# Kernel tuning notes

Measured on AMD Instinct MI355X. Metric: run time of the kernel, lower is better.

Reference implementation:

```python
import jax, jax.numpy as jnp
import numpy as np

N_AGENTS = 8
STATE_DIM = 256
EMBED_DIM = 32
BATCH = 65536


def setup_inputs() -> dict:
    key = jax.random.key(0)
    ks = jax.random.split(key, 12)
    s = 1.0 / np.sqrt(STATE_DIM)
    se = 1.0 / np.sqrt(EMBED_DIM)
    return {
        "agent_qs": jax.random.normal(ks[0], (BATCH, N_AGENTS), dtype=jnp.float32),
        "states": jax.random.normal(ks[1], (BATCH, STATE_DIM), dtype=jnp.float32),
        # hyper_w_1: Linear(state_dim, embed_dim * n_agents)
        "w1_W": jax.random.uniform(ks[2], (STATE_DIM, EMBED_DIM * N_AGENTS), jnp.float32, -s, s),
        "w1_b": jax.random.uniform(ks[3], (EMBED_DIM * N_AGENTS,), jnp.float32, -s, s),
        # hyper_w_final: Linear(state_dim, embed_dim)
        "wf_W": jax.random.uniform(ks[4], (STATE_DIM, EMBED_DIM), jnp.float32, -s, s),
        "wf_b": jax.random.uniform(ks[5], (EMBED_DIM,), jnp.float32, -s, s),
        # hyper_b_1: Linear(state_dim, embed_dim)
        "b1_W": jax.random.uniform(ks[6], (STATE_DIM, EMBED_DIM), jnp.float32, -s, s),
        "b1_b": jax.random.uniform(ks[7], (EMBED_DIM,), jnp.float32, -s, s),
        # V: Linear(state_dim, embed_dim) -> ReLU -> Linear(embed_dim, 1)
        "v1_W": jax.random.uniform(ks[8], (STATE_DIM, EMBED_DIM), jnp.float32, -s, s),
        "v1_b": jax.random.uniform(ks[9], (EMBED_DIM,), jnp.float32, -s, s),
        "v2_W": jax.random.uniform(ks[10], (EMBED_DIM, 1), jnp.float32, -se, se),
        "v2_b": jax.random.uniform(ks[11], (1,), jnp.float32, -se, se),
    }


def reference(agent_qs, states, w1_W, w1_b, wf_W, wf_b, b1_W, b1_b, v1_W, v1_b, v2_W, v2_b):
    B = agent_qs.shape[0]
    # hypernet weights (abs for monotonicity)
    w1 = jnp.abs(states @ w1_W + w1_b).reshape(B, N_AGENTS, EMBED_DIM)   # [B, A, E]
    w_final = jnp.abs(states @ wf_W + wf_b)                               # [B, E]
    b1 = states @ b1_W + b1_b                                             # [B, E]
    # hidden = elu(agent_qs^T w1 + b1): [B,1,A] @ [B,A,E] -> [B,E]
    hidden = jax.nn.elu(jnp.einsum("ba,bae->be", agent_qs, w1) + b1)
    # mixed = hidden @ w_final: [B,1,E] @ [B,E,1] -> [B,1]
    mixed = jnp.sum(hidden * w_final, axis=-1, keepdims=True)             # [B, 1]
    # state value V(s)
    state_value = jax.nn.relu(states @ v1_W + v1_b) @ v2_W + v2_b         # [B, 1]
    return mixed + state_value
```

## Files before the change

kernel.cpp:

```cpp
#include <hip/hip_runtime.h>
#include <math.h>


#define NTILES 22
#define KCHUNKS 8
#define CHUNK_I4 1408

typedef __attribute__((ext_vector_type(8))) short short8;
typedef __attribute__((ext_vector_type(4))) float float4v;

__device__ __forceinline__ unsigned short f2b(float f) {
    unsigned int u = __float_as_uint(f);
    u = u + 0x7fffu + ((u >> 16) & 1u);
    return (unsigned short)(u >> 16);
}

__device__ __forceinline__ void gl2lds16(const unsigned short* g, unsigned short* l) {
    __builtin_amdgcn_global_load_lds(
        (const __attribute__((address_space(1))) unsigned int*)g,
        (__attribute__((address_space(3))) unsigned int*)l,
        16, 0, 0);
}

__global__ void repack_b(const float* __restrict__ w1_W,
                         const float* __restrict__ wf_W,
                         const float* __restrict__ b1_W,
                         const float* __restrict__ v1_W,
                         unsigned short* __restrict__ brep) {
    int idx = blockIdx.x * 256 + threadIdx.x;
    int lane = idx & 63;
    int tt   = idx >> 6;
    int t    = tt % 22;
    int kc   = tt / 22;
    int kbase = kc * 32 + (lane >> 4) * 8;
    int n = t * 16 + (lane & 15);
    short8 frag;
#pragma unroll
    for (int j = 0; j < 8; ++j) {
        int k = kbase + j;
        float val;
        if (n < 256)      val = w1_W[k * 256 + n];
        else if (n < 288) val = wf_W[k * 32 + (n - 256)];
        else if (n < 320) val = b1_W[k * 32 + (n - 288)];
        else              val = v1_W[k * 32 + (n - 320)];
        frag[j] = (short)f2b(val);
    }
    *(short8*)(&brep[idx * 8]) = frag;
}

__global__ void __launch_bounds__(256, 2)
qmix_main(const float* __restrict__ agent_qs,
          const float* __restrict__ states,
          const unsigned short* __restrict__ brep,
          const float* __restrict__ w1_b,
          const float* __restrict__ wf_b,
          const float* __restrict__ b1_b,
          const float* __restrict__ v1_b,
          const float* __restrict__ v2_W,
          const float* __restrict__ v2_b,
          float* __restrict__ out) {
    __shared__ __align__(16) unsigned short wlds[2][NTILES * 64 * 8];

    const int tid  = threadIdx.x;
    const int wave = tid >> 6, lane = tid & 63;
    const int quad = lane >> 4, l16 = lane & 15;
    const int r0 = blockIdx.x * 128 + wave * 32 + l16;
    const float* srow0 = states + (size_t)r0 * 256;
    const float* srow1 = srow0 + 16 * 256;

    for (int s = wave; s < NTILES; s += 4)
        gl2lds16(brep + (size_t)(s * 64 + lane) * 8, wlds[0] + s * 512);

    float4v s0a = *(const float4v*)(srow0 + quad * 8);
    float4v s0b = *(const float4v*)(srow0 + quad * 8 + 4);
    float4v s1a = *(const float4v*)(srow1 + quad * 8);
    float4v s1b = *(const float4v*)(srow1 + quad * 8 + 4);

    float4v acc[2][NTILES];
#pragma unroll
    for (int g = 0; g < 2; ++g)
#pragma unroll
        for (int t = 0; t < NTILES; ++t)
#pragma unroll
            for (int q = 0; q < 4; ++q) acc[g][t][q] = 0.f;

    __syncthreads();

    int cur = 0;
    for (int kc = 0; kc < KCHUNKS; ++kc) {
        if (kc < KCHUNKS - 1) {
            const unsigned short* src = brep + (size_t)(kc + 1) * CHUNK_I4 * 8;
            unsigned short* dst = wlds[cur ^ 1];
            for (int s = wave; s < NTILES; s += 4)
                gl2lds16(src + (size_t)(s * 64 + lane) * 8, dst + s * 512);
        }
        short8 b0, b1;
#pragma unroll
        for (int j = 0; j < 4; ++j) {
            b0[j] = (short)f2b(s0a[j]); b0[4 + j] = (short)f2b(s0b[j]);
            b1[j] = (short)f2b(s1a[j]); b1[4 + j] = (short)f2b(s1b[j]);
        }
        if (kc < KCHUNKS - 1) {
            const float* p0 = srow0 + (kc + 1) * 32 + quad * 8;
            const float* p1 = srow1 + (kc + 1) * 32 + quad * 8;
            s0a = *(const float4v*)(p0);
            s0b = *(const float4v*)(p0 + 4);
            s1a = *(const float4v*)(p1);
            s1b = *(const float4v*)(p1 + 4);
        }
        const short8* wb = (const short8*)wlds[cur] + lane;
#pragma unroll
        for (int t = 0; t < NTILES; ++t) {
            short8 af = wb[t * 64];
            acc[0][t] = __builtin_amdgcn_mfma_f32_16x16x32_bf16(af, b0, acc[0][t], 0, 0, 0);
            acc[1][t] = __builtin_amdgcn_mfma_f32_16x16x32_bf16(af, b1, acc[1][t], 0, 0, 0);
        }
        cur ^= 1;
        __syncthreads();
    }

#pragma unroll
    for (int g = 0; g < 2; ++g) {
        const int row = r0 + g * 16;
        float4v q0 = *(const float4v*)(agent_qs + (size_t)row * 8);
        float4v q1 = *(const float4v*)(agent_qs + (size_t)row * 8 + 4);
        float qv[8] = {q0[0], q0[1], q0[2], q0[3], q1[0], q1[1], q1[2], q1[3]};

        float qacc[8], wfv[8], b1v[8], svp = 0.f;
#pragma unroll
        for (int s = 0; s < 8; ++s) qacc[s] = 0.f;

#pragma unroll
        for (int t = 0; t < NTILES; ++t) {
            const float* bptr =
                (t < 16) ? (w1_b + t * 16) :
                (t < 18) ? (wf_b + (t - 16) * 16) :
                (t < 20) ? (b1_b + (t - 18) * 16) : (v1_b + (t - 20) * 16);
            float4v bb = *(const float4v*)(bptr + quad * 4);
            float vb[4];
#pragma unroll
            for (int j = 0; j < 4; ++j) vb[j] = acc[g][t][j] + bb[j];

            if (t < 16) {
                float q = qv[t >> 1];
                int base = (t & 1) * 4;
#pragma unroll
                for (int j = 0; j < 4; ++j) qacc[base + j] += q * fabsf(vb[j]);
            } else if (t < 18) {
                int base = (t - 16) * 4;
#pragma unroll
                for (int j = 0; j < 4; ++j) wfv[base + j] = fabsf(vb[j]);
            } else if (t < 20) {
                int base = (t - 18) * 4;
#pragma unroll
                for (int j = 0; j < 4; ++j) b1v[base + j] = vb[j];
            } else {
                int ebase = (t - 20) * 16 + quad * 4;
#pragma unroll
                for (int j = 0; j < 4; ++j)
                    svp += fmaxf(vb[j], 0.f) * v2_W[ebase + j];
            }
        }

        float mix = 0.f;
#pragma unroll
        for (int s = 0; s < 8; ++s) {
            float h = qacc[s] + b1v[s];
            h = h > 0.f ? h : (__expf(h) - 1.f);
            mix += h * wfv[s];
        }
        float tot = mix + svp;
        tot += __shfl_xor(tot, 16);
        tot += __shfl_xor(tot, 32);
        if (quad == 0) out[row] = tot + v2_b[0];
    }
}

extern "C" void kernel_launch(void* const* d_in, const int* in_sizes, int n_in,
                              void* d_out, int out_size, void* d_ws, size_t ws_size,
                              hipStream_t stream) {
    const float* agent_qs = (const float*)d_in[0];
    const float* states   = (const float*)d_in[1];
    const float* w1_W = (const float*)d_in[2];
    const float* w1_b = (const float*)d_in[3];
    const float* wf_W = (const float*)d_in[4];
    const float* wf_b = (const float*)d_in[5];
    const float* b1_W = (const float*)d_in[6];
    const float* b1_b = (const float*)d_in[7];
    const float* v1_W = (const float*)d_in[8];
    const float* v1_b = (const float*)d_in[9];
    const float* v2_W = (const float*)d_in[10];
    const float* v2_b = (const float*)d_in[11];
    float* out = (float*)d_out;
    unsigned short* brep = (unsigned short*)d_ws;

    repack_b<<<44, 256, 0, stream>>>(w1_W, wf_W, b1_W, v1_W, brep);
    qmix_main<<<512, 256, 0, stream>>>(agent_qs, states, brep,
                                       w1_b, wf_b, b1_b, v1_b, v2_W, v2_b, out);
}
```

Measured before the change: 127.2 us.

## Deepen LDS prefetch pipeline with explicit vmcnt waits and split barriers

Issues the DMA for two weight chunks ahead and the states loads through inline asm. A __syncthreads is replaced with explicit s_waitcnt vmcnt counts tuned per wave (waves 0-1 issue 6 tile DMAs, waves 2-3 issue 5), so a wave waits only for the chunk it needs while later loads stay in flight. The k-loop is fully unrolled. The hand-counted vmcnt values are fragile: if the compiler emits any other vector-memory op, or the instruction order changes, the waits become wrong and race. Register pressure from unrolling may also rise.

```diff
diff --git a/kernel.cpp b/kernel.cpp
--- a/kernel.cpp
+++ b/kernel.cpp
@@ -20,6 +20,12 @@
         (const __attribute__((address_space(1))) unsigned int*)g,
         (__attribute__((address_space(3))) unsigned int*)l,
         16, 0, 0);
+}
+
+__device__ __forceinline__ float4v ld16_async(const float* p) {
+    float4v r;
+    asm volatile("global_load_dwordx4 %0, %1, off" : "=v"(r) : "v"(p));
+    return r;
 }
 
 __global__ void repack_b(const float* __restrict__ w1_W,
@@ -68,13 +74,27 @@
     const float* srow0 = states + (size_t)r0 * 256;
     const float* srow1 = srow0 + 16 * 256;
 
-    for (int s = wave; s < NTILES; s += 4)
-        gl2lds16(brep + (size_t)(s * 64 + lane) * 8, wlds[0] + s * 512);
-
-    float4v s0a = *(const float4v*)(srow0 + quad * 8);
-    float4v s0b = *(const float4v*)(srow0 + quad * 8 + 4);
-    float4v s1a = *(const float4v*)(srow1 + quad * 8);
-    float4v s1b = *(const float4v*)(srow1 + quad * 8 + 4);
+    float4v st[4];
+
+#define ISSUE_STATES(kcv) do {                                          \
+        const float* p0_ = srow0 + (kcv) * 32 + quad * 8;               \
+        const float* p1_ = srow1 + (kcv) * 32 + quad * 8;               \
+        st[0] = ld16_async(p0_);                                        \
+        st[1] = ld16_async(p0_ + 4);                                    \
+        st[2] = ld16_async(p1_);                                        \
+        st[3] = ld16_async(p1_ + 4);                                    \
+    } while (0)
+
+#define ISSUE_DMA(kcv, bufv) do {                                       \
+        const unsigned short* src_ = brep + (size_t)(kcv) * CHUNK_I4 * 8; \
+        unsigned short* dst_ = wlds[bufv];                              \
+        for (int s_ = wave; s_ < NTILES; s_ += 4)                       \
+            gl2lds16(src_ + (size_t)(s_ * 64 + lane) * 8, dst_ + s_ * 512); \
+    } while (0)
+
+    ISSUE_DMA(0, 0);
+    ISSUE_STATES(0);
+    ISSUE_DMA(1, 1);
 
     float4v acc[2][NTILES];
 #pragma unroll
@@ -84,39 +104,45 @@
 #pragma unroll
             for (int q = 0; q < 4; ++q) acc[g][t][q] = 0.f;
 
-    __syncthreads();
-
-    int cur = 0;
+#pragma unroll
     for (int kc = 0; kc < KCHUNKS; ++kc) {
-        if (kc < KCHUNKS - 1) {
-            const unsigned short* src = brep + (size_t)(kc + 1) * CHUNK_I4 * 8;
-            unsigned short* dst = wlds[cur ^ 1];
-            for (int s = wave; s < NTILES; s += 4)
-                gl2lds16(src + (size_t)(s * 64 + lane) * 8, dst + s * 512);
-        }
+        const int buf = kc & 1;
+
+        if (kc == KCHUNKS - 1)
+            asm volatile("s_waitcnt vmcnt(0)" ::: "memory");
+        else if (wave < 2)
+            asm volatile("s_waitcnt vmcnt(6)" ::: "memory");
+        else
+            asm volatile("s_waitcnt vmcnt(5)" ::: "memory");
+        __builtin_amdgcn_sched_barrier(0);
+        __builtin_amdgcn_s_barrier();
+        __builtin_amdgcn_sched_barrier(0);
+
         short8 b0, b1;
 #pragma unroll
         for (int j = 0; j < 4; ++j) {
-            b0[j] = (short)f2b(s0a[j]); b0[4 + j] = (short)f2b(s0b[j]);
-            b1[j] = (short)f2b(s1a[j]); b1[4 + j] = (short)f2b(s1b[j]);
-        }
-        if (kc < KCHUNKS - 1) {
-            const float* p0 = srow0 + (kc + 1) * 32 + quad * 8;
-            const float* p1 = srow1 + (kc + 1) * 32 + quad * 8;
-            s0a = *(const float4v*)(p0);
-            s0b = *(const float4v*)(p0 + 4);
-            s1a = *(const float4v*)(p1);
-            s1b = *(const float4v*)(p1 + 4);
-        }
-        const short8* wb = (const short8*)wlds[cur] + lane;
+            b0[j]     = (short)f2b(st[0][j]);
+            b0[4 + j] = (short)f2b(st[1][j]);
+            b1[j]     = (short)f2b(st[2][j]);
+            b1[4 + j] = (short)f2b(st[3][j]);
+        }
+        if (kc + 1 < KCHUNKS) ISSUE_STATES(kc + 1);
+
+        const short8* wb = (const short8*)wlds[buf] + lane;
 #pragma unroll
         for (int t = 0; t < NTILES; ++t) {
             short8 af = wb[t * 64];
             acc[0][t] = __builtin_amdgcn_mfma_f32_16x16x32_bf16(af, b0, acc[0][t], 0, 0, 0);
             acc[1][t] = __builtin_amdgcn_mfma_f32_16x16x32_bf16(af, b1, acc[1][t], 0, 0, 0);
         }
-        cur ^= 1;
-        __syncthreads();
+
+        if (kc + 2 < KCHUNKS) {
+            asm volatile("s_waitcnt lgkmcnt(0)" ::: "memory");
+            __builtin_amdgcn_sched_barrier(0);
+            __builtin_amdgcn_s_barrier();
+            __builtin_amdgcn_sched_barrier(0);
+            ISSUE_DMA(kc + 2, buf);
+        }
     }
 
 #pragma unroll
```

Measured after the change: 127.1 us. No clear change (-0.1%).

## Split output tiles across wave pairs to halve accumulators and raise occupancy

Applied to the files above, without the earlier changes.

Each block now handles 64 rows instead of 128, and each pair of waves splits the 22 output tiles in half, 11 tiles per wave. This halves the accumulator registers, so launch bounds can go up to 4 blocks per SM, and the grid doubles to 1024 blocks. The LDS weight buffer is single-buffered, so each chunk now needs an extra barrier and loses the previous prefetch overlap. Partial agent sums are exchanged through LDS between the two halves before the epilogue. This trades pipelining and extra syncs plus twice the weight traffic per row for higher occupancy.

```diff
diff --git a/kernel.cpp b/kernel.cpp
--- a/kernel.cpp
+++ b/kernel.cpp
@@ -48,7 +48,7 @@
     *(short8*)(&brep[idx * 8]) = frag;
 }
 
-__global__ void __launch_bounds__(256, 2)
+__global__ void __launch_bounds__(256, 4)
 qmix_main(const float* __restrict__ agent_qs,
           const float* __restrict__ states,
           const unsigned short* __restrict__ brep,
@@ -59,65 +59,61 @@
           const float* __restrict__ v2_W,
           const float* __restrict__ v2_b,
           float* __restrict__ out) {
-    __shared__ __align__(16) unsigned short wlds[2][NTILES * 64 * 8];
+    __shared__ __align__(16) unsigned short wlds[NTILES * 64 * 8];
 
     const int tid  = threadIdx.x;
     const int wave = tid >> 6, lane = tid & 63;
     const int quad = lane >> 4, l16 = lane & 15;
-    const int r0 = blockIdx.x * 128 + wave * 32 + l16;
-    const float* srow0 = states + (size_t)r0 * 256;
+    const int pair = wave >> 1;
+    const int half = wave & 1;
+    const int tbase = half * 11;
+    const int r0 = blockIdx.x * 64 + pair * 32 + l16;
+    const float* srow0 = states + (size_t)r0 * 256 + quad * 8;
     const float* srow1 = srow0 + 16 * 256;
 
-    for (int s = wave; s < NTILES; s += 4)
-        gl2lds16(brep + (size_t)(s * 64 + lane) * 8, wlds[0] + s * 512);
-
-    float4v s0a = *(const float4v*)(srow0 + quad * 8);
-    float4v s0b = *(const float4v*)(srow0 + quad * 8 + 4);
-    float4v s1a = *(const float4v*)(srow1 + quad * 8);
-    float4v s1b = *(const float4v*)(srow1 + quad * 8 + 4);
-
-    float4v acc[2][NTILES];
+    float4v acc[2][11];
 #pragma unroll
     for (int g = 0; g < 2; ++g)
 #pragma unroll
-        for (int t = 0; t < NTILES; ++t)
-#pragma unroll
-            for (int q = 0; q < 4; ++q) acc[g][t][q] = 0.f;
+        for (int i = 0; i < 11; ++i)
+#pragma unroll
+            for (int q = 0; q < 4; ++q) acc[g][i][q] = 0.f;
+
+#pragma unroll
+    for (int kc = 0; kc < KCHUNKS; ++kc) {
+        if (kc) __syncthreads();
+
+        const unsigned short* src = brep + (size_t)kc * CHUNK_I4 * 8;
+        for (int s = wave; s < NTILES; s += 4)
+            gl2lds16(src + (size_t)(s * 64 + lane) * 8, wlds + s * 512);
+
+        float4v s0a = *(const float4v*)(srow0 + kc * 32);
+        float4v s0b = *(const float4v*)(srow0 + kc * 32 + 4);
+        float4v s1a = *(const float4v*)(srow1 + kc * 32);
+        float4v s1b = *(const float4v*)(srow1 + kc * 32 + 4);
+
+        __syncthreads();
+
+        short8 b0, b1;
+#pragma unroll
+        for (int j = 0; j < 4; ++j) {
+            b0[j]     = (short)f2b(s0a[j]);
+            b0[4 + j] = (short)f2b(s0b[j]);
+            b1[j]     = (short)f2b(s1a[j]);
+            b1[4 + j] = (short)f2b(s1b[j]);
+        }
+
+        const short8* wb = (const short8*)wlds + lane;
+#pragma unroll
+        for (int i = 0; i < 11; ++i) {
+            short8 af = wb[(tbase + i) * 64];
+            acc[0][i] = __builtin_amdgcn_mfma_f32_16x16x32_bf16(af, b0, acc[0][i], 0, 0, 0);
+            acc[1][i] = __builtin_amdgcn_mfma_f32_16x16x32_bf16(af, b1, acc[1][i], 0, 0, 0);
+        }
+    }
 
     __syncthreads();
-
-    int cur = 0;
-    for (int kc = 0; kc < KCHUNKS; ++kc) {
-        if (kc < KCHUNKS - 1) {
-            const unsigned short* src = brep + (size_t)(kc + 1) * CHUNK_I4 * 8;
-            unsigned short* dst = wlds[cur ^ 1];
-            for (int s = wave; s < NTILES; s += 4)
-                gl2lds16(src + (size_t)(s * 64 + lane) * 8, dst + s * 512);
-        }
-        short8 b0, b1;
-#pragma unroll
-        for (int j = 0; j < 4; ++j) {
-            b0[j] = (short)f2b(s0a[j]); b0[4 + j] = (short)f2b(s0b[j]);
-            b1[j] = (short)f2b(s1a[j]); b1[4 + j] = (short)f2b(s1b[j]);
-        }
-        if (kc < KCHUNKS - 1) {
-            const float* p0 = srow0 + (kc + 1) * 32 + quad * 8;
-            const float* p1 = srow1 + (kc + 1) * 32 + quad * 8;
-            s0a = *(const float4v*)(p0);
-            s0b = *(const float4v*)(p0 + 4);
-            s1a = *(const float4v*)(p1);
-            s1b = *(const float4v*)(p1 + 4);
-        }
-        const short8* wb = (const short8*)wlds[cur] + lane;
-#pragma unroll
-        for (int t = 0; t < NTILES; ++t) {
-            short8 af = wb[t * 64];
-            acc[0][t] = __builtin_amdgcn_mfma_f32_16x16x32_bf16(af, b0, acc[0][t], 0, 0, 0);
-            acc[1][t] = __builtin_amdgcn_mfma_f32_16x16x32_bf16(af, b1, acc[1][t], 0, 0, 0);
-        }
-        cur ^= 1;
-        __syncthreads();
-    }
+    float* scr = (float*)wlds;
 
 #pragma unroll
     for (int g = 0; g < 2; ++g) {
@@ -128,10 +124,11 @@
 
         float qacc[8], wfv[8], b1v[8], svp = 0.f;
 #pragma unroll
-        for (int s = 0; s < 8; ++s) qacc[s] = 0.f;
-
-#pragma unroll
-        for (int t = 0; t < NTILES; ++t) {
+        for (int s = 0; s < 8; ++s) { qacc[s] = 0.f; wfv[s] = 0.f; b1v[s] = 0.f; }
+
+#pragma unroll
+        for (int i = 0; i < 11; ++i) {
+            const int t = tbase + i;
             const float* bptr =
                 (t < 16) ? (w1_b + t * 16) :
                 (t < 18) ? (wf_b + (t - 16) * 16) :
@@ -139,7 +136,7 @@
             float4v bb = *(const float4v*)(bptr + quad * 4);
             float vb[4];
 #pragma unroll
-            for (int j = 0; j < 4; ++j) vb[j] = acc[g][t][j] + bb[j];
+            for (int j = 0; j < 4; ++j) vb[j] = acc[g][i][j] + bb[j];
 
             if (t < 16) {
                 float q = qv[t >> 1];
@@ -162,17 +159,28 @@
             }
         }
 
-        float mix = 0.f;
-#pragma unroll
-        for (int s = 0; s < 8; ++s) {
-            float h = qacc[s] + b1v[s];
-            h = h > 0.f ? h : (__expf(h) - 1.f);
-            mix += h * wfv[s];
-        }
-        float tot = mix + svp;
-        tot += __shfl_xor(tot, 16);
-        tot += __shfl_xor(tot, 32);
-        if (quad == 0) out[row] = tot + v2_b[0];
+        float* reg = scr + (size_t)(pair * 2 + g) * 512 + lane * 8;
+        if (half == 0) {
+            *(float4v*)(reg)     = *(float4v*)(qacc);
+            *(float4v*)(reg + 4) = *(float4v*)(qacc + 4);
+        }
+        __syncthreads();
+        if (half == 1) {
+            float4v pa = *(const float4v*)(reg);
+            float4v pb = *(const float4v*)(reg + 4);
+            float mix = 0.f;
+#pragma unroll
+            for (int s = 0; s < 8; ++s) {
+                float qs = qacc[s] + ((s < 4) ? pa[s] : pb[s - 4]);
+                float h = qs + b1v[s];
+                h = h > 0.f ? h : (__expf(h) - 1.f);
+                mix += h * wfv[s];
+            }
+            float tot = mix + svp;
+            tot += __shfl_xor(tot, 16);
+            tot += __shfl_xor(tot, 32);
+            if (quad == 0) out[row] = tot + v2_b[0];
+        }
     }
 }
 
@@ -195,6 +203,6 @@
     unsigned short* brep = (unsigned short*)d_ws;
 
     repack_b<<<44, 256, 0, stream>>>(w1_W, wf_W, b1_W, v1_W, brep);
-    qmix_main<<<512, 256, 0, stream>>>(agent_qs, states, brep,
-                                       w1_b, wf_b, b1_b, v1_b, v2_W, v2_b, out);
-}
+    qmix_main<<<1024, 256, 0, stream>>>(agent_qs, states, brep,
+                                        w1_b, wf_b, b1_b, v1_b, v2_W, v2_b, out);
+}
```

Result: slower. 167.7 us (+31.8%).

## Stream weight fragments from global/L2 into registers instead of LDS double buffer

Applied to the files above, without the earlier changes.

Drops the LDS double-buffered weight staging, its global_load_lds copies and the per-chunk __syncthreads. Each wave now loads its bf16 weight fragments straight from global memory (an L2-resident 22 KB-per-chunk table) into a 4-deep register prefetch ring. The K loop is fully unrolled via a macro with ping-pong state buffers. Removing barriers and LDS traffic trades for more per-wave global/L2 load traffic and extra VGPR pressure, which could affect occupancy.

```diff
diff --git a/kernel.cpp b/kernel.cpp
--- a/kernel.cpp
+++ b/kernel.cpp
@@ -4,7 +4,7 @@
 
 #define NTILES 22
 #define KCHUNKS 8
-#define CHUNK_I4 1408
+#define NSLOTS 176
 
 typedef __attribute__((ext_vector_type(8))) short short8;
 typedef __attribute__((ext_vector_type(4))) float float4v;
@@ -13,13 +13,6 @@
     unsigned int u = __float_as_uint(f);
     u = u + 0x7fffu + ((u >> 16) & 1u);
     return (unsigned short)(u >> 16);
-}
-
-__device__ __forceinline__ void gl2lds16(const unsigned short* g, unsigned short* l) {
-    __builtin_amdgcn_global_load_lds(
-        (const __attribute__((address_space(1))) unsigned int*)g,
-        (__attribute__((address_space(3))) unsigned int*)l,
-        16, 0, 0);
 }
 
 __global__ void repack_b(const float* __restrict__ w1_W,
@@ -59,22 +52,23 @@
           const float* __restrict__ v2_W,
           const float* __restrict__ v2_b,
           float* __restrict__ out) {
-    __shared__ __align__(16) unsigned short wlds[2][NTILES * 64 * 8];
-
     const int tid  = threadIdx.x;
     const int wave = tid >> 6, lane = tid & 63;
     const int quad = lane >> 4, l16 = lane & 15;
     const int r0 = blockIdx.x * 128 + wave * 32 + l16;
-    const float* srow0 = states + (size_t)r0 * 256;
+    const float* srow0 = states + (size_t)r0 * 256 + quad * 8;
     const float* srow1 = srow0 + 16 * 256;
 
-    for (int s = wave; s < NTILES; s += 4)
-        gl2lds16(brep + (size_t)(s * 64 + lane) * 8, wlds[0] + s * 512);
+    const short8* fp = (const short8*)brep + lane;
 
-    float4v s0a = *(const float4v*)(srow0 + quad * 8);
-    float4v s0b = *(const float4v*)(srow0 + quad * 8 + 4);
-    float4v s1a = *(const float4v*)(srow1 + quad * 8);
-    float4v s1b = *(const float4v*)(srow1 + quad * 8 + 4);
+    float4v stA[4], stB[4];
+    stA[0] = *(const float4v*)(srow0);
+    stA[1] = *(const float4v*)(srow0 + 4);
+    stA[2] = *(const float4v*)(srow1);
+    stA[3] = *(const float4v*)(srow1 + 4);
+
+    short8 f[4];
+    f[0] = fp[0 * 64]; f[1] = fp[1 * 64]; f[2] = fp[2 * 64]; f[3] = fp[3 * 64];
 
     float4v acc[2][NTILES];
 #pragma unroll
@@ -84,40 +78,40 @@
 #pragma unroll
             for (int q = 0; q < 4; ++q) acc[g][t][q] = 0.f;
 
-    __syncthreads();
+#define CHUNK(kcv, CUR, NXT) do {                                           \
+        short8 b0, b1;                                                      \
+        _Pragma("unroll")                                                   \
+        for (int j = 0; j < 4; ++j) {                                       \
+            b0[j]     = (short)f2b(CUR[0][j]);                              \
+            b0[4 + j] = (short)f2b(CUR[1][j]);                              \
+            b1[j]     = (short)f2b(CUR[2][j]);                              \
+            b1[4 + j] = (short)f2b(CUR[3][j]);                              \
+        }                                                                   \
+        if ((kcv) + 1 < KCHUNKS) {                                          \
+            NXT[0] = *(const float4v*)(srow0 + ((kcv) + 1) * 32);           \
+            NXT[1] = *(const float4v*)(srow0 + ((kcv) + 1) * 32 + 4);       \
+            NXT[2] = *(const float4v*)(srow1 + ((kcv) + 1) * 32);           \
+            NXT[3] = *(const float4v*)(srow1 + ((kcv) + 1) * 32 + 4);       \
+        }                                                                   \
+        _Pragma("unroll")                                                   \
+        for (int t = 0; t < NTILES; ++t) {                                  \
+            const int ti = (kcv) * NTILES + t;                              \
+            short8 af = f[ti & 3];                                          \
+            if (ti + 4 < NSLOTS) f[ti & 3] = fp[(size_t)(ti + 4) * 64];     \
+            acc[0][t] = __builtin_amdgcn_mfma_f32_16x16x32_bf16(af, b0, acc[0][t], 0, 0, 0); \
+            acc[1][t] = __builtin_amdgcn_mfma_f32_16x16x32_bf16(af, b1, acc[1][t], 0, 0, 0); \
+        }                                                                   \
+    } while (0)
 
-    int cur = 0;
-    for (int kc = 0; kc < KCHUNKS; ++kc) {
-        if (kc < KCHUNKS - 1) {
-            const unsigned short* src = brep + (size_t)(kc + 1) * CHUNK_I4 * 8;
-            unsigned short* dst = wlds[cur ^ 1];
-            for (int s = wave; s < NTILES; s += 4)
-                gl2lds16(src + (size_t)(s * 64 + lane) * 8, dst + s * 512);
-        }
-        short8 b0, b1;
-#pragma unroll
-        for (int j = 0; j < 4; ++j) {
-            b0[j] = (short)f2b(s0a[j]); b0[4 + j] = (short)f2b(s0b[j]);
-            b1[j] = (short)f2b(s1a[j]); b1[4 + j] = (short)f2b(s1b[j]);
-        }
-        if (kc < KCHUNKS - 1) {
-            const float* p0 = srow0 + (kc + 1) * 32 + quad * 8;
-            const float* p1 = srow1 + (kc + 1) * 32 + quad * 8;
-            s0a = *(const float4v*)(p0);
-            s0b = *(const float4v*)(p0 + 4);
-            s1a = *(const float4v*)(p1);
-            s1b = *(const float4v*)(p1 + 4);
-        }
-        const short8* wb = (const short8*)wlds[cur] + lane;
-#pragma unroll
-        for (int t = 0; t < NTILES; ++t) {
-            short8 af = wb[t * 64];
-            acc[0][t] = __builtin_amdgcn_mfma_f32_16x16x32_bf16(af, b0, acc[0][t], 0, 0, 0);
-            acc[1][t] = __builtin_amdgcn_mfma_f32_16x16x32_bf16(af, b1, acc[1][t], 0, 0, 0);
-        }
-        cur ^= 1;
-        __syncthreads();
-    }
+    CHUNK(0, stA, stB);
+    CHUNK(1, stB, stA);
+    CHUNK(2, stA, stB);
+    CHUNK(3, stB, stA);
+    CHUNK(4, stA, stB);
+    CHUNK(5, stB, stA);
+    CHUNK(6, stA, stB);
+    CHUNK(7, stB, stA);
+#undef CHUNK
 
 #pragma unroll
     for (int g = 0; g < 2; ++g) {
```

After: 163.8 us. 1.29x slower.
